# Kernel optimization log

Measured on AMD Instinct MI355X. Metric: run time of the kernel, lower is better.

Reference implementation:

```python
import jax, jax.numpy as jnp
import numpy as np

MIN_RAD, MAX_RAD, EPS = 0.9, 0.999, 1e-8


def block_diag_linear(x, w, b):
    # x: [B, T, H*bw], w: [H, bw, bw], b: [H, bw]
    h, bw, _ = w.shape
    xb = x.reshape(x.shape[0], x.shape[1], h, bw)
    y = jnp.einsum('bthi,hij->bthj', xb, w) + b
    return y.reshape(x.shape)


def setup_inputs() -> dict:
    key = jax.random.key(0)
    kx, kw1, kw2, ka = jax.random.split(key, 4)
    B, T, width, num_heads = 8, 4096, 1024, 8
    bw = width // num_heads
    std = np.sqrt(1.0 / bw)
    x = jax.random.normal(kx, (B, T, width), dtype=jnp.float32)
    ig_w = std * jax.random.normal(kw1, (num_heads, bw, bw), dtype=jnp.float32)
    ig_b = jnp.zeros((num_heads, bw), dtype=jnp.float32)
    ag_w = std * jax.random.normal(kw2, (num_heads, bw, bw), dtype=jnp.float32)
    ag_b = jnp.zeros((num_heads, bw), dtype=jnp.float32)
    # rnn_param_init: u ~ U(min_rad^2+eps, max_rad^2+eps); a_param = log(exp(-0.5*log u) - 1)
    u = jax.random.uniform(ka, (width,), dtype=jnp.float32,
                           minval=MIN_RAD**2 + EPS, maxval=MAX_RAD**2 + EPS)
    a_param = jnp.log(jnp.exp(-0.5 * jnp.log(u)) - 1.0)
    return {"x": x, "ig_w": ig_w, "ig_b": ig_b, "ag_w": ag_w, "ag_b": ag_b,
            "a_param": a_param}


def reference(x, ig_w, ig_b, ag_w, ag_b, a_param):
    gate_x = jax.nn.sigmoid(block_diag_linear(x, ig_w, ig_b))
    gate_a = jax.nn.sigmoid(block_diag_linear(x, ag_w, ag_b))
    log_a = -8.0 * gate_a * jax.nn.softplus(a_param)  # [B, T, D]
    a = jnp.exp(log_a)
    a2 = jnp.exp(2.0 * log_a)
    gated_x = x * gate_x
    multiplier = jnp.sqrt(jnp.clip(1.0 - a2, 1e-7))
    normed_x = gated_x * multiplier
    # closed-form diagonal scan: h_t = a_t * h_{t-1} + normed_x_t, h_{-1}=0
    B, T, D = x.shape
    p = jnp.cumprod(a, axis=1)
    p_prefix = jnp.concatenate([jnp.ones((B, 1, D), x.dtype), p[:, :-1]], axis=1)
    p_prefix = jnp.clip(p_prefix, 1e-7)
    w = normed_x / p_prefix
    S = jnp.cumsum(w, axis=1)
    h = p_prefix * S  # h0 = 0 so alpha term vanishes
    return h
```

## Files before the change

kernel.cpp:

```cpp
#include <hip/hip_runtime.h>
#include <math.h>

#define B_   8
#define T_   4096
#define D_   1024
#define H_   8
#define BW_  128
#define TC_  32
#define NC_  (T_/TC_)
#define NT_  8

typedef __attribute__((ext_vector_type(8)))  short bf16x8;
typedef __attribute__((ext_vector_type(16))) float f32x16;
typedef __attribute__((ext_vector_type(4)))  unsigned short u16x4;

__device__ __forceinline__ unsigned short f2bf(float f) {
    unsigned int u = __float_as_uint(f);
    unsigned int r = (u + 0x7fffu + ((u >> 16) & 1u)) >> 16;
    return (unsigned short)r;
}
__device__ __forceinline__ float bf2f(unsigned short h) {
    return __uint_as_float(((unsigned int)h) << 16);
}
__device__ __forceinline__ float fast_exp(float x) {
    return __builtin_amdgcn_exp2f(x * 1.4426950408889634f);
}
__device__ __forceinline__ float fast_rcp(float x) {
    return __builtin_amdgcn_rcpf(x);
}
__device__ __forceinline__ float fast_sqrt(float x) {
    return __builtin_amdgcn_sqrtf(x);
}
__device__ __forceinline__ float up_n(unsigned int u)  {
    return __uint_as_float(u & 0xffff0000u);
}
__device__ __forceinline__ float up_a(unsigned int u)  {
    return fast_exp(__uint_as_float(u << 16));
}

__global__ __launch_bounds__(256) void k0_wprep(
    const float* __restrict__ igw, const float* __restrict__ agw,
    unsigned short* __restrict__ wtIh, unsigned short* __restrict__ wtIl,
    unsigned short* __restrict__ wtAh, unsigned short* __restrict__ wtAl)
{
    const int h   = blockIdx.x >> 3;
    const int seg = blockIdx.x & 7;
    const float* wi = igw + ((size_t)h << 14);
    const float* wa = agw + ((size_t)h << 14);
    #pragma unroll
    for (int j = 0; j < 8; ++j) {
        int idx = seg * 2048 + threadIdx.x + 256 * j;
        int k = idx >> 7, c = idx & 127;
        int o = (h << 14) + (c << 7) + k;
        float vI = wi[idx], vA = wa[idx];
        unsigned short ih = f2bf(vI); unsigned short il = f2bf(vI - bf2f(ih));
        unsigned short ah = f2bf(vA); unsigned short al = f2bf(vA - bf2f(ah));
        wtIh[o] = ih; wtIl[o] = il; wtAh[o] = ah; wtAl[o] = al;
    }
}

__global__ __launch_bounds__(256, 2) void k1_gates_mfma(
    const float* __restrict__ x,
    const unsigned short* __restrict__ wtIh, const unsigned short* __restrict__ wtIl,
    const unsigned short* __restrict__ wtAh, const unsigned short* __restrict__ wtAl,
    const float* __restrict__ igb, const float* __restrict__ agb,
    const float* __restrict__ ap,
    unsigned int* __restrict__ anArr, float* __restrict__ PA)
{
    __shared__ unsigned short xs_hi[64][128];
    __shared__ unsigned short xs_lo[64][128];

    const int tg0 = blockIdx.x;
    const int h   = blockIdx.y;
    const int b   = blockIdx.z;
    const int tid = threadIdx.x;

    const int cb = tid >> 6;
    const int l  = tid & 63;
    const int lr = l & 31;
    const int hl = l >> 5;

    const size_t wtoff = ((size_t)h << 14) + (size_t)(cb * 32 + lr) * 128 + hl * 8;
    const unsigned short* pIh = wtIh + wtoff;
    const unsigned short* pIl = wtIl + wtoff;
    const unsigned short* pAh = wtAh + wtoff;
    const unsigned short* pAl = wtAl + wtoff;
    bf16x8 fIh[8], fIl[8], fAh[8], fAl[8];
    #pragma unroll
    for (int ks = 0; ks < 8; ++ks) {
        fIh[ks] = *(const bf16x8*)(pIh + ks * 16);
        fIl[ks] = *(const bf16x8*)(pIl + ks * 16);
        fAh[ks] = *(const bf16x8*)(pAh + ks * 16);
        fAl[ks] = *(const bf16x8*)(pAl + ks * 16);
    }

    const int d = h * BW_ + cb * 32 + lr;
    const float bI = igb[d], bA = agb[d];
    const float sp = log1pf(expf(ap[d]));

    for (int nt = 0; nt < NT_; ++nt) {
        const int tc = tg0 * NT_ + nt;
        const int t0 = tc * 64;

        const float* xbase = x + ((size_t)b * T_ + t0) * D_ + h * BW_;
        #pragma unroll
        for (int i = 0; i < 8; ++i) {
            int idx = tid + 256 * i;
            int row = idx >> 5, c4 = idx & 31;
            float4 v = *(const float4*)(xbase + (size_t)row * D_ + c4 * 4);
            int col0 = (c4 * 4) ^ ((row & 7) << 3);
            u16x4 hv, lv;
            hv.x = f2bf(v.x); lv.x = f2bf(v.x - bf2f(hv.x));
            hv.y = f2bf(v.y); lv.y = f2bf(v.y - bf2f(hv.y));
            hv.z = f2bf(v.z); lv.z = f2bf(v.z - bf2f(hv.z));
            hv.w = f2bf(v.w); lv.w = f2bf(v.w - bf2f(hv.w));
            *(u16x4*)&xs_hi[row][col0] = hv;
            *(u16x4*)&xs_lo[row][col0] = lv;
        }
        __syncthreads();

        f32x16 aI0, aI1, aA0, aA1;
        #pragma unroll
        for (int i = 0; i < 16; ++i) { aI0[i]=0.f; aI1[i]=0.f; aA0[i]=0.f; aA1[i]=0.f; }

        #pragma unroll
        for (int ks = 0; ks < 8; ++ks) {
            const int k0 = ks * 16 + hl * 8;
            const int kk = k0 ^ ((lr & 7) << 3);
            bf16x8 xh0 = *(const bf16x8*)&xs_hi[lr][kk];
            bf16x8 xl0 = *(const bf16x8*)&xs_lo[lr][kk];
            bf16x8 xh1 = *(const bf16x8*)&xs_hi[32 + lr][kk];
            bf16x8 xl1 = *(const bf16x8*)&xs_lo[32 + lr][kk];

            aI0 = __builtin_amdgcn_mfma_f32_32x32x16_bf16(xh0, fIh[ks], aI0, 0, 0, 0);
            aI0 = __builtin_amdgcn_mfma_f32_32x32x16_bf16(xl0, fIh[ks], aI0, 0, 0, 0);
            aI0 = __builtin_amdgcn_mfma_f32_32x32x16_bf16(xh0, fIl[ks], aI0, 0, 0, 0);

            aI1 = __builtin_amdgcn_mfma_f32_32x32x16_bf16(xh1, fIh[ks], aI1, 0, 0, 0);
            aI1 = __builtin_amdgcn_mfma_f32_32x32x16_bf16(xl1, fIh[ks], aI1, 0, 0, 0);
            aI1 = __builtin_amdgcn_mfma_f32_32x32x16_bf16(xh1, fIl[ks], aI1, 0, 0, 0);

            aA0 = __builtin_amdgcn_mfma_f32_32x32x16_bf16(xh0, fAh[ks], aA0, 0, 0, 0);
            aA0 = __builtin_amdgcn_mfma_f32_32x32x16_bf16(xl0, fAh[ks], aA0, 0, 0, 0);
            aA0 = __builtin_amdgcn_mfma_f32_32x32x16_bf16(xh0, fAl[ks], aA0, 0, 0, 0);

            aA1 = __builtin_amdgcn_mfma_f32_32x32x16_bf16(xh1, fAh[ks], aA1, 0, 0, 0);
            aA1 = __builtin_amdgcn_mfma_f32_32x32x16_bf16(xl1, fAh[ks], aA1, 0, 0, 0);
            aA1 = __builtin_amdgcn_mfma_f32_32x32x16_bf16(xh1, fAl[ks], aA1, 0, 0, 0);
        }

        const size_t obase = ((size_t)b * T_ + t0) * D_ + d;
        float pr0 = 1.f, pr1 = 1.f;
        #pragma unroll
        for (int tg = 0; tg < 2; ++tg) {
            #pragma unroll
            for (int r = 0; r < 16; ++r) {
                float yI = (tg ? aI1[r] : aI0[r]) + bI;
                float yA = (tg ? aA1[r] : aA0[r]) + bA;
                int row = (r & 3) + ((r >> 2) << 3) + 4 * hl;
                float gx = fast_rcp(1.f + fast_exp(-yI));
                float ga = fast_rcp(1.f + fast_exp(-yA));
                float la = -8.f * ga * sp;
                unsigned short lab = f2bf(la);
                float av = fast_exp(bf2f(lab));
                float mu = fast_sqrt(fmaxf(1.f - av * av, 1e-7f));
                int colx = (cb * 32 + lr) ^ ((row & 7) << 3);
                int rg = tg * 32 + row;
                float xv = bf2f(xs_hi[rg][colx]) + bf2f(xs_lo[rg][colx]);
                float nv = xv * gx * mu;
                if (tg) pr1 *= av; else pr0 *= av;
                anArr[obase + (size_t)rg * D_] =
                    ((unsigned int)f2bf(nv) << 16) | lab;
            }
        }
        float q0 = pr0 * __shfl_xor(pr0, 32, 64);
        float q1 = pr1 * __shfl_xor(pr1, 32, 64);
        if (hl == 0) {
            PA[((size_t)(tc * 2)     * B_ + b) * D_ + d] = q0;
            PA[((size_t)(tc * 2 + 1) * B_ + b) * D_ + d] = q1;
        }
        __syncthreads();
    }
}

__global__ void k2_pin(const float* __restrict__ PA, float* __restrict__ Pin)
{
    int id = blockIdx.x * 256 + threadIdx.x;
    float P = 1.f;
    for (int cidx = 0; cidx < NC_; ++cidx) {
        Pin[(size_t)cidx * B_ * D_ + id] = P;
        P *= PA[(size_t)cidx * B_ * D_ + id];
    }
}

__global__ __launch_bounds__(256) void k3_wsum(
    const unsigned int* __restrict__ anArr,
    const float* __restrict__ Pin, float* __restrict__ Wsum)
{
    const int cidx = blockIdx.x, b = blockIdx.y;
    const int tid = threadIdx.x;
    float P[4], W[4];
    #pragma unroll
    for (int j = 0; j < 4; ++j) {
        P[j] = Pin[((size_t)cidx * B_ + b) * D_ + tid + 256 * j];
        W[j] = 0.f;
    }
    const size_t base = ((size_t)b * T_ + cidx * TC_) * D_ + tid;
    for (int i = 0; i < TC_; ++i) {
        #pragma unroll
        for (int j = 0; j < 4; ++j) {
            size_t o = base + (size_t)i * D_ + 256 * j;
            unsigned int u = anArr[o];
            float n = up_n(u);
            float a = up_a(u);
            float pp = fmaxf(P[j], 1e-7f);
            W[j] += n / pp;
            P[j] *= a;
        }
    }
    #pragma unroll
    for (int j = 0; j < 4; ++j)
        Wsum[((size_t)cidx * B_ + b) * D_ + tid + 256 * j] = W[j];
}

__global__ void k4_sin(const float* __restrict__ Wsum, float* __restrict__ Sin)
{
    int id = blockIdx.x * 256 + threadIdx.x;
    float S = 0.f;
    for (int cidx = 0; cidx < NC_; ++cidx) {
        Sin[(size_t)cidx * B_ * D_ + id] = S;
        S += Wsum[(size_t)cidx * B_ * D_ + id];
    }
}

__global__ __launch_bounds__(256) void k5_final(
    const unsigned int* __restrict__ anArr,
    const float* __restrict__ Pin, const float* __restrict__ Sin,
    float* __restrict__ hOut)
{
    const int cidx = blockIdx.x, b = blockIdx.y;
    const int tid = threadIdx.x;
    float P[4], S[4];
    #pragma unroll
    for (int j = 0; j < 4; ++j) {
        P[j] = Pin[((size_t)cidx * B_ + b) * D_ + tid + 256 * j];
        S[j] = Sin[((size_t)cidx * B_ + b) * D_ + tid + 256 * j];
    }
    const size_t base = ((size_t)b * T_ + cidx * TC_) * D_ + tid;
    for (int i = 0; i < TC_; ++i) {
        #pragma unroll
        for (int j = 0; j < 4; ++j) {
            size_t o = base + (size_t)i * D_ + 256 * j;
            unsigned int u = anArr[o];
            float n = up_n(u);
            float a = up_a(u);
            float pp = fmaxf(P[j], 1e-7f);
            float w = n / pp;
            S[j] += w;
            hOut[o] = pp * S[j];
            P[j] *= a;
        }
    }
}

__global__ void k_sentinel(float* out, float v)
{
    if (threadIdx.x == 0 && blockIdx.x == 0) out[0] = v;
}

extern "C" void kernel_launch(void* const* d_in, const int* in_sizes, int n_in,
                              void* d_out, int out_size, void* d_ws, size_t ws_size,
                              hipStream_t stream)
{
    const float* x   = (const float*)d_in[0];
    const float* igw = (const float*)d_in[1];
    const float* igb = (const float*)d_in[2];
    const float* agw = (const float*)d_in[3];
    const float* agb = (const float*)d_in[4];
    const float* ap  = (const float*)d_in[5];
    float* hOut = (float*)d_out;

    const size_t elems = (size_t)B_ * T_ * D_;
    const size_t agg   = (size_t)NC_ * B_ * D_;
    const size_t needB = (elems + 4 * agg) * sizeof(float);

    if (ws_size < needB) {
        k_sentinel<<<1, 64, 0, stream>>>(hOut, (float)ws_size);
        return;
    }

    unsigned int* anArr = (unsigned int*)d_ws;
    float* PA   = (float*)(anArr + elems);
    float* Pin  = PA   + agg;
    float* Wsum = Pin  + agg;
    float* Sin  = Wsum + agg;

    unsigned short* wtIh = (unsigned short*)Pin;
    unsigned short* wtIl = wtIh + 131072;
    unsigned short* wtAh = wtIl + 131072;
    unsigned short* wtAl = wtAh + 131072;

    k0_wprep<<<dim3(64), 256, 0, stream>>>(igw, agw, wtIh, wtIl, wtAh, wtAl);

    dim3 g1(T_ / 64 / NT_, H_, B_);
    k1_gates_mfma<<<g1, 256, 0, stream>>>(x, wtIh, wtIl, wtAh, wtAl,
                                          igb, agb, ap, anArr, PA);

    k2_pin<<<dim3((B_ * D_) / 256), 256, 0, stream>>>(PA, Pin);

    k3_wsum<<<dim3(NC_, B_), 256, 0, stream>>>(anArr, Pin, Wsum);

    k4_sin<<<dim3((B_ * D_) / 256), 256, 0, stream>>>(Wsum, Sin);

    k5_final<<<dim3(NC_, B_), 256, 0, stream>>>(anArr, Pin, Sin, hOut);
}
```

Before: 184.9 us.

## Compute per-chunk weighted sums in gate kernel to skip full rescan in k3

The gate kernel now also computes, for each 32-step chunk, the local prefix-scaled sum of normed inputs (Ac) and their plain sum (Bc), using shuffles to combine band products across the two half-waves. k3 then derives each chunk's weighted sum from these aggregates with one division in the common case, instead of re-reading all 32 packed elements. It falls back to the serial rescan only when the clamp at 1e-7 applies partway through a chunk. This removes most of the full-tensor read in k3, at the cost of extra arithmetic and two more aggregate writes in k1, plus different rounding from using unrounded values.

```diff
diff --git a/kernel.cpp b/kernel.cpp
--- a/kernel.cpp
+++ b/kernel.cpp
@@ -65,7 +65,8 @@
     const unsigned short* __restrict__ wtAh, const unsigned short* __restrict__ wtAl,
     const float* __restrict__ igb, const float* __restrict__ agb,
     const float* __restrict__ ap,
-    unsigned int* __restrict__ anArr, float* __restrict__ PA)
+    unsigned int* __restrict__ anArr, float* __restrict__ PA,
+    float* __restrict__ Ac, float* __restrict__ Bc)
 {
     __shared__ unsigned short xs_hi[64][128];
     __shared__ unsigned short xs_lo[64][128];
@@ -151,10 +152,14 @@
 
         const size_t obase = ((size_t)b * T_ + t0) * D_ + d;
         float pr0 = 1.f, pr1 = 1.f;
+        float AcOut[2], BcOut[2];
         #pragma unroll
         for (int tg = 0; tg < 2; ++tg) {
+            float bandP[4], bandS[4];
+            float wbp = 1.f, sumN = 0.f;
             #pragma unroll
             for (int r = 0; r < 16; ++r) {
+                const int j = r >> 2, i = r & 3;
                 float yI = (tg ? aI1[r] : aI0[r]) + bI;
                 float yA = (tg ? aA1[r] : aA0[r]) + bA;
                 int row = (r & 3) + ((r >> 2) << 3) + 4 * hl;
@@ -169,15 +174,36 @@
                 float xv = bf2f(xs_hi[rg][colx]) + bf2f(xs_lo[rg][colx]);
                 float nv = xv * gx * mu;
                 if (tg) pr1 *= av; else pr0 *= av;
+                if (i == 0) { wbp = 1.f; bandS[j] = nv; }
+                else        { bandS[j] += nv * fast_rcp(wbp); }
+                wbp *= av;
+                if (i == 3) bandP[j] = wbp;
+                sumN += nv;
                 anArr[obase + (size_t)rg * D_] =
                     ((unsigned int)f2bf(nv) << 16) | lab;
             }
+            float oB0 = __shfl_xor(bandP[0], 32, 64);
+            float oB1 = __shfl_xor(bandP[1], 32, 64);
+            float oB2 = __shfl_xor(bandP[2], 32, 64);
+            float oB3 = __shfl_xor(bandP[3], 32, 64);
+            float m1 = bandP[0], m2 = m1 * bandP[1], m3 = m2 * bandP[2];
+            float o1 = oB0, o2 = o1 * oB1, o3 = o2 * oB2, o4 = o3 * oB3;
+            float p0, p1, p2, p3;
+            if (hl == 0) { p0 = 1.f; p1 = m1 * o1; p2 = m2 * o2; p3 = m3 * o3; }
+            else         { p0 = o1;  p1 = m1 * o2; p2 = m2 * o3; p3 = m3 * o4; }
+            float Apart = bandS[0] * fast_rcp(p0) + bandS[1] * fast_rcp(p1)
+                        + bandS[2] * fast_rcp(p2) + bandS[3] * fast_rcp(p3);
+            AcOut[tg] = Apart + __shfl_xor(Apart, 32, 64);
+            BcOut[tg] = sumN  + __shfl_xor(sumN, 32, 64);
         }
         float q0 = pr0 * __shfl_xor(pr0, 32, 64);
         float q1 = pr1 * __shfl_xor(pr1, 32, 64);
         if (hl == 0) {
-            PA[((size_t)(tc * 2)     * B_ + b) * D_ + d] = q0;
-            PA[((size_t)(tc * 2 + 1) * B_ + b) * D_ + d] = q1;
+            size_t c0 = ((size_t)(tc * 2)     * B_ + b) * D_ + d;
+            size_t c1 = ((size_t)(tc * 2 + 1) * B_ + b) * D_ + d;
+            PA[c0] = q0;        PA[c1] = q1;
+            Ac[c0] = AcOut[0];  Ac[c1] = AcOut[1];
+            Bc[c0] = BcOut[0];  Bc[c1] = BcOut[1];
         }
         __syncthreads();
     }
@@ -194,33 +220,38 @@
 }
 
 __global__ __launch_bounds__(256) void k3_wsum(
-    const unsigned int* __restrict__ anArr,
-    const float* __restrict__ Pin, float* __restrict__ Wsum)
+    const unsigned int* __restrict__ anArr, const float* __restrict__ Pin,
+    const float* __restrict__ PAc, const float* __restrict__ Ac,
+    const float* __restrict__ Bc, float* __restrict__ Wsum)
 {
     const int cidx = blockIdx.x, b = blockIdx.y;
     const int tid = threadIdx.x;
-    float P[4], W[4];
+    const size_t aggb = ((size_t)cidx * B_ + b) * D_ + tid;
     #pragma unroll
     for (int j = 0; j < 4; ++j) {
-        P[j] = Pin[((size_t)cidx * B_ + b) * D_ + tid + 256 * j];
-        W[j] = 0.f;
-    }
-    const size_t base = ((size_t)b * T_ + cidx * TC_) * D_ + tid;
-    for (int i = 0; i < TC_; ++i) {
-        #pragma unroll
-        for (int j = 0; j < 4; ++j) {
-            size_t o = base + (size_t)i * D_ + 256 * j;
-            unsigned int u = anArr[o];
-            float n = up_n(u);
-            float a = up_a(u);
-            float pp = fmaxf(P[j], 1e-7f);
-            W[j] += n / pp;
-            P[j] *= a;
-        }
-    }
-    #pragma unroll
-    for (int j = 0; j < 4; ++j)
-        Wsum[((size_t)cidx * B_ + b) * D_ + tid + 256 * j] = W[j];
+        const size_t ai = aggb + 256 * j;
+        float P  = Pin[ai];
+        float pa = PAc[ai];
+        float W;
+        if (P < 1e-7f) {
+            W = Bc[ai] * 1e7f;
+        } else if (P * pa >= 1e-7f) {
+            W = Ac[ai] / P;
+        } else {
+            W = 0.f;
+            float Pt = P;
+            const size_t base = ((size_t)b * T_ + cidx * TC_) * D_ + tid + 256 * j;
+            for (int i = 0; i < TC_; ++i) {
+                unsigned int u = anArr[base + (size_t)i * D_];
+                float n = up_n(u);
+                float a = up_a(u);
+                float pp = fmaxf(Pt, 1e-7f);
+                W += n / pp;
+                Pt *= a;
+            }
+        }
+        Wsum[ai] = W;
+    }
 }
 
 __global__ void k4_sin(const float* __restrict__ Wsum, float* __restrict__ Sin)
@@ -282,7 +313,7 @@
 
     const size_t elems = (size_t)B_ * T_ * D_;
     const size_t agg   = (size_t)NC_ * B_ * D_;
-    const size_t needB = (elems + 4 * agg) * sizeof(float);
+    const size_t needB = (elems + 6 * agg) * sizeof(float);
 
     if (ws_size < needB) {
         k_sentinel<<<1, 64, 0, stream>>>(hOut, (float)ws_size);
@@ -294,6 +325,8 @@
     float* Pin  = PA   + agg;
     float* Wsum = Pin  + agg;
     float* Sin  = Wsum + agg;
+    float* Ac   = Sin  + agg;
+    float* Bc   = Ac   + agg;
 
     unsigned short* wtIh = (unsigned short*)Pin;
     unsigned short* wtIl = wtIh + 131072;
@@ -304,11 +337,11 @@
 
     dim3 g1(T_ / 64 / NT_, H_, B_);
     k1_gates_mfma<<<g1, 256, 0, stream>>>(x, wtIh, wtIl, wtAh, wtAl,
-                                          igb, agb, ap, anArr, PA);
+                                          igb, agb, ap, anArr, PA, Ac, Bc);
 
     k2_pin<<<dim3((B_ * D_) / 256), 256, 0, stream>>>(PA, Pin);
 
-    k3_wsum<<<dim3(NC_, B_), 256, 0, stream>>>(anArr, Pin, Wsum);
+    k3_wsum<<<dim3(NC_, B_), 256, 0, stream>>>(anArr, Pin, PA, Ac, Bc, Wsum);
 
     k4_sin<<<dim3((B_ * D_) / 256), 256, 0, stream>>>(Wsum, Sin);
 
```

New measurement: 222.4 us. 20.3% more time.
